# Kernel optimization log

Hardware: AMD Instinct MI355X
Metric: run time of the kernel (lower is better)

Reference implementation:

```python
import jax, jax.numpy as jnp
import numpy as np

B, L, D_MODEL, D_K, HEADS, C = 4, 4096, 512, 64, 8, 2
TOPK = int(C * np.log(L))  # int(c * log(input_seq_len)) = 16


def setup_inputs() -> dict:
    key = jax.random.key(0)
    ks = jax.random.split(key, 5)
    q_in = jax.random.normal(ks[0], (B, L, D_MODEL), jnp.float32)
    k_in = jax.random.normal(ks[1], (B, L, D_MODEL), jnp.float32)
    v_in = jax.random.normal(ks[2], (B, L, D_MODEL), jnp.float32)
    Wq = jax.random.normal(ks[3], (D_MODEL, D_K), jnp.float32) / np.sqrt(D_MODEL)
    bq = jax.random.normal(ks[4], (D_K,), jnp.float32) * 0.01
    return {"q_in": q_in, "k_in": k_in, "v_in": v_in, "Wq": Wq, "bq": bq}


def _to_heads(x, Wq, bq):
    # Faithful to original: ALL of q/k/v use the `query` Dense layer, and all
    # heads are identical copies (same projection stacked `heads` times).
    p = x @ Wq + bq                       # [B, L, d_k]
    p = jnp.swapaxes(p, 1, 2)             # [B, d_k, L]  (transpose [0,3,2,1] of [B,L,d,H])
    return jnp.broadcast_to(p[:, None], (p.shape[0], HEADS, D_K, p.shape[-1]))  # [B,H,d,L]


def reference(q_in, k_in, v_in, Wq, bq):
    Q = jnp.fft.fft(_to_heads(q_in, Wq, bq).astype(jnp.complex64), axis=-1)
    K = jnp.fft.fft(_to_heads(k_in, Wq, bq).astype(jnp.complex64), axis=-1)
    V = _to_heads(v_in, Wq, bq)           # [B,H,d,L] float32
    QK = jnp.fft.ifft(Q * jnp.conj(K), axis=-1)   # circular cross-correlation
    qk_abs = jnp.abs(QK)                  # [B,H,d,L]

    vals, idx = jax.lax.top_k(qk_abs, TOPK)       # [B,H,d,k]
    w = jax.nn.softmax(vals, axis=-1)             # softmax over the k lags

    # tf.roll(v, shift=-lag): out[t] = v[(t + lag) mod L]  -> vectorized gather
    t = jnp.arange(L, dtype=jnp.int32)
    gidx = (idx[..., None] + t) % L               # [B,H,d,k,L]
    Vk = jnp.broadcast_to(V[:, :, :, None, :], gidx.shape)
    rolled = jnp.take_along_axis(Vk, gidx, axis=-1)           # [B,H,d,k,L]
    agg = jnp.sum(rolled * w[..., None], axis=3)              # [B,H,d,L]

    out = agg.reshape(agg.shape[0], HEADS * D_K, L)           # [B, H*d, L]
    return jnp.transpose(out, (0, 2, 1))                      # [B, L, H*d]
```

## Files before the change

kernel.cpp:

```cpp
#include <hip/hip_runtime.h>
#include <hip/hip_bf16.h>

#define BQ 4
#define LQ 4096
#define DM 512
#define DK 64
#define NROWS (BQ * DK)
#define TOPK 16
#define CAND 32

typedef __attribute__((ext_vector_type(4))) float f32x4;
typedef __attribute__((ext_vector_type(8))) short short8v;
typedef __attribute__((ext_vector_type(16))) float f32x16;

__device__ __forceinline__ unsigned short f2bf(float x) {
  unsigned u = __builtin_bit_cast(unsigned, x);
  return (unsigned short)((u + 0x7FFFu + ((u >> 16) & 1u)) >> 16);
}
__device__ __forceinline__ float bf2f(unsigned short h) {
  unsigned u = ((unsigned)h) << 16;
  return __builtin_bit_cast(float, u);
}

__device__ __forceinline__ void gl_lds16(const float* g, float* s) {
  auto g1 = (const __attribute__((address_space(1))) float*)(uintptr_t)g;
  auto s3 = (__attribute__((address_space(3))) float*)(uint32_t)(uintptr_t)s;
  __builtin_amdgcn_global_load_lds(g1, s3, 16, 0, 0);
}

__device__ __forceinline__ void mfma_drain() {
  __builtin_amdgcn_sched_barrier(0);
  asm volatile("s_nop 7\n\ts_nop 7\n\ts_nop 7\n\ts_nop 7" ::: "memory");
  __builtin_amdgcn_sched_barrier(0);
}

#define VMCNT(n)                                            \
  do {                                                      \
    asm volatile("s_waitcnt vmcnt(" #n ")" ::: "memory");   \
    __builtin_amdgcn_sched_barrier(0);                      \
  } while (0)

__global__ __launch_bounds__(256) void wprep_kernel(
    const float* __restrict__ Wq, short* __restrict__ wpack) {
  const int ks = blockIdx.x;
  const int t = threadIdx.x;
  const int lane = t & 63, half = t >> 6;
  const int plane = half >> 1, nt = half & 1;
  const int r = nt * 32 + (lane & 31);
  const int kb = 16 * ks + 8 * (lane >> 5);
  short8v o;
#pragma unroll
  for (int i = 0; i < 8; ++i) {
    float v = Wq[(size_t)(kb + i) * DK + r];
    unsigned short h = f2bf(v);
    o[i] = plane ? (short)f2bf(v - bf2f(h)) : (short)h;
  }
  *(short8v*)(&wpack[(((size_t)plane * 2 + nt) * 32 + ks) * 512 + lane * 8]) = o;
}

#define WLOADR(buf, ksg_)                                                      \
  do {                                                                         \
    const short* wb_ = wp0 + ((size_t)(ksg_) << 9);                            \
    asm volatile("global_load_dwordx4 %0, %1, off" : "=v"(buf[0]) : "v"(wb_)); \
    asm volatile("global_load_dwordx4 %0, %1, off" : "=v"(buf[1]) : "v"(wb_ + (64 << 9))); \
    asm volatile("global_load_dwordx4 %0, %1, off" : "=v"(buf[2]) : "v"(wb_ + (32 << 9))); \
    asm volatile("global_load_dwordx4 %0, %1, off" : "=v"(buf[3]) : "v"(wb_ + (96 << 9))); \
  } while (0)

__global__ __launch_bounds__(256, 2) void proj_kernel(
    const float* __restrict__ q_in, const float* __restrict__ k_in,
    const float* __restrict__ v_in, const short* __restrict__ wpack,
    const float* __restrict__ bq, float* __restrict__ ws) {
  const float* x = blockIdx.z == 0 ? q_in : (blockIdx.z == 1 ? k_in : v_in);
  float* outp = ws + (size_t)blockIdx.z * (size_t)(NROWS * LQ);

  __shared__ __align__(16) float xs[16384];

  const int tid = threadIdx.x;
  const int l = tid & 63, wv = tid >> 6;
  const int r = l & 31, hi = l >> 5;
  const int R0 = blockIdx.x * 32;

  float* slice = xs + wv * 4096;

  {
    const float* xw = x + (size_t)R0 * DM + 128 * wv;
#pragma unroll
    for (int j = 0; j < 16; ++j) {
      const int row = 2 * j + hi;
      const float* src = xw + (size_t)row * DM + ((r ^ (row & 7)) << 2);
      gl_lds16(src, slice + j * 256);
    }
  }

  const short* wp0 = wpack + l * 8;
  short8v wr3[3][4];
  WLOADR(wr3[0], 8 * wv + 0);
  WLOADR(wr3[1], 8 * wv + 1);

  f32x16 acc[2];
#pragma unroll
  for (int nt = 0; nt < 2; ++nt)
#pragma unroll
    for (int i = 0; i < 16; ++i) acc[nt][i] = 0.f;

  const float* rbase = slice + r * 128;
  const int c = r & 7;

#pragma unroll
  for (int kl = 0; kl < 8; ++kl) {
    if (kl < 6) WLOADR(wr3[(kl + 2) % 3], 8 * wv + kl + 2);
    if (kl < 6) VMCNT(8);
    else if (kl == 6) VMCNT(4);
    else VMCNT(0);

    const int q0 = 4 * kl + 2 * hi;
    f32x4 xa = *(const f32x4*)(rbase + ((q0 ^ c) << 2));
    f32x4 xb2 = *(const f32x4*)(rbase + (((q0 + 1) ^ c) << 2));
    float f[8] = {xa[0], xa[1], xa[2], xa[3], xb2[0], xb2[1], xb2[2], xb2[3]};
    short8v ah, al;
#pragma unroll
    for (int i = 0; i < 8; ++i) {
      unsigned short h = f2bf(f[i]);
      ah[i] = (short)h;
      al[i] = (short)f2bf(f[i] - bf2f(h));
    }
    short8v* w_ = wr3[kl % 3];
    asm volatile(
        "s_nop 4\n\t"
        "v_mfma_f32_32x32x16_bf16 %0, %2, %4, %0\n\t"
        "v_mfma_f32_32x32x16_bf16 %0, %2, %5, %0\n\t"
        "v_mfma_f32_32x32x16_bf16 %0, %3, %4, %0\n\t"
        "v_mfma_f32_32x32x16_bf16 %1, %2, %6, %1\n\t"
        "v_mfma_f32_32x32x16_bf16 %1, %2, %7, %1\n\t"
        "v_mfma_f32_32x32x16_bf16 %1, %3, %6, %1\n\t"
        "s_nop 7\n\t"
        "s_nop 3"
        : "+v"(acc[0]), "+v"(acc[1])
        : "v"(ah), "v"(al), "v"(w_[0]), "v"(w_[1]), "v"(w_[2]), "v"(w_[3]));
  }

  mfma_drain();
#pragma unroll
  for (int nt = 0; nt < 2; ++nt)
#pragma unroll
    for (int rr = 0; rr < 16; ++rr)
      slice[nt * 1024 + rr * 64 + l] = acc[nt][rr];
  __syncthreads();

  if (wv < 2) {
    const int nt = wv;
    float sacc[16];
#pragma unroll
    for (int rr = 0; rr < 16; ++rr)
      sacc[rr] = xs[0 * 4096 + nt * 1024 + rr * 64 + l] +
                 xs[1 * 4096 + nt * 1024 + rr * 64 + l] +
                 xs[2 * 4096 + nt * 1024 + rr * 64 + l] +
                 xs[3 * 4096 + nt * 1024 + rr * 64 + l];
    float* area = xs + wv * 4096 + 2048;
    const float bb = bq[nt * 32 + r];
#pragma unroll
    for (int rr = 0; rr < 16; ++rr) {
      int io = (rr & 3) + 8 * (rr >> 2) + 4 * hi;
      area[r * 34 + io] = sacc[rr] + bb;
    }
    asm volatile("s_waitcnt lgkmcnt(0)" ::: "memory");
    __builtin_amdgcn_sched_barrier(0);
    const int e = l & 15, jg = l >> 4;
    const int b = R0 >> 12, i0 = R0 & (LQ - 1);
#pragma unroll
    for (int p = 0; p < 8; ++p) {
      int jj = jg * 8 + p;
      float2 v = *reinterpret_cast<const float2*>(area + jj * 34 + e * 2);
      *reinterpret_cast<float2*>(
          &outp[((size_t)b * DK + nt * 32 + jj) * LQ + i0 + e * 2]) = v;
    }
  }
}

__global__ __launch_bounds__(512) void corr_topk_kernel(
    const float* __restrict__ qp, const float* __restrict__ kp,
    float* __restrict__ lw) {
  const int row = blockIdx.x;
  const int tid = threadIdx.x;
  __shared__ __align__(16) short qs[3 * 4112 + 4096];
  __shared__ __align__(16) short ks[4096];
  __shared__ __align__(16) float qf[LQ];
  __shared__ __align__(16) float kf[LQ];
  __shared__ unsigned wk[128];
  __shared__ unsigned scand[CAND];
  __shared__ float rS[CAND];
  __shared__ float ordv[TOPK]; __shared__ int ordl[TOPK];

  const float* qr = qp + ((size_t)row << 12);
  const float* kr = kp + ((size_t)row << 12);

  {
    const float4* q4 = (const float4*)qr;
    float4 v0 = q4[tid * 2], v1 = q4[tid * 2 + 1];
    float4 v2 = q4[(tid * 2 + 2) & 1023];
    ((float4*)qf)[tid * 2] = v0;
    ((float4*)qf)[tid * 2 + 1] = v1;
    float f[12] = {v0.x, v0.y, v0.z, v0.w, v1.x, v1.y, v1.z, v1.w,
                   v2.x, v2.y, v2.z, v2.w};
#pragma unroll
    for (int r = 0; r < 4; ++r) {
      short8v o;
#pragma unroll
      for (int i = 0; i < 8; ++i) o[i] = (short)f2bf(f[i + r]);
      *(short8v*)(&qs[r * 4112 + tid * 8]) = o;
    }
    const float4* k4 = (const float4*)kr;
    float4 w0 = k4[tid * 2], w1 = k4[tid * 2 + 1];
    ((float4*)kf)[tid * 2] = w0;
    ((float4*)kf)[tid * 2 + 1] = w1;
    float g[8] = {w0.x, w0.y, w0.z, w0.w, w1.x, w1.y, w1.z, w1.w};
    int Q = tid;
    int Qs = Q ^ ((Q >> 3) & 7);
    short8v o;
#pragma unroll
    for (int i = 0; i < 8; ++i) o[i] = (short)f2bf(g[i]);
    *(short8v*)(&ks[Qs << 3]) = o;
  }
  __syncthreads();

  const int l = tid & 63, wv = tid >> 6;
  const int Oq = ((8 * (l >> 5) - 32 * (l & 31)) & 4095) >> 3;
  const int rB = (l & 31) & 3;
  const int Ce = (l & 31) + 8 * (l >> 5) - rB;
  const short* qb = qs + rB * 4112;

  f32x16 acc[4];
#pragma unroll
  for (int M = 0; M < 4; ++M)
#pragma unroll
    for (int i = 0; i < 16; ++i) acc[M][i] = 0.f;

  const int J0 = wv * 32;
#pragma unroll 2
  for (int jb = 0; jb < 32; ++jb) {
    const int J = J0 + jb;
    int e1 = (Ce + 16 * J) & 4095;
    int e2 = (e1 + 4) & 4095;
    uint2 blo = *(const uint2*)(qb + e1);
    uint2 bhi = *(const uint2*)(qb + e2);
    int4 bi; bi.x = blo.x; bi.y = blo.y; bi.z = bhi.x; bi.w = bhi.y;
    short8v bf = __builtin_bit_cast(short8v, bi);
    const int Dq = 2 * J;
#pragma unroll
    for (int M = 0; M < 4; ++M) {
      int Q = (Oq + Dq - 128 * M) & 511;
      Q ^= (Q >> 3) & 7;
      short8v af = *(const short8v*)(&ks[Q << 3]);
      asm volatile("v_mfma_f32_32x32x16_bf16 %0, %1, %2, %0"
                   : "+v"(acc[M]) : "v"(af), "v"(bf));
    }
  }

  mfma_drain();
  __syncthreads();
  float* red = (float*)qs;
  const int strip = (wv & 1) * 4096;
  const int ch4 = (l >> 5) * 4, cn = l & 31;
#define RIDX(M, r) (strip + ((M) << 10) + 32 * (((r)&3) + 8 * ((r) >> 2) + ch4) + cn)
  if (wv < 2) {
#pragma unroll
    for (int M = 0; M < 4; ++M)
#pragma unroll
      for (int r = 0; r < 16; ++r) red[RIDX(M, r)] = acc[M][r];
  }
  __syncthreads();
  if (wv >= 2 && wv < 4) {
#pragma unroll
    for (int M = 0; M < 4; ++M)
#pragma unroll
      for (int r = 0; r < 16; ++r) red[RIDX(M, r)] += acc[M][r];
  }
  __syncthreads();
  if (wv >= 4 && wv < 6) {
#pragma unroll
    for (int M = 0; M < 4; ++M)
#pragma unroll
      for (int r = 0; r < 16; ++r) red[RIDX(M, r)] += acc[M][r];
  }
  __syncthreads();
  if (wv >= 6) {
#pragma unroll
    for (int M = 0; M < 4; ++M)
#pragma unroll
      for (int r = 0; r < 16; ++r) red[RIDX(M, r)] += acc[M][r];
  }
  __syncthreads();
#undef RIDX

  {
    unsigned key[8];
#pragma unroll
    for (int i = 0; i < 8; ++i) {
      int tau = wv * 512 + i * 64 + l;
      float v = red[tau] + red[4096 + tau];
      unsigned u = __builtin_bit_cast(unsigned, fabsf(v));
      key[i] = (u & 0xFFFFF000u) | (unsigned)(4095 - tau);
    }
    unsigned bkey = key[0];
#pragma unroll
    for (int i = 1; i < 8; ++i) bkey = key[i] > bkey ? key[i] : bkey;
    for (int round = 0; round < 16; ++round) {
      unsigned m = bkey;
#pragma unroll
      for (int off = 1; off < 64; off <<= 1) {
        unsigned o = __shfl_xor(m, off);
        m = o > m ? o : m;
      }
      if (l == 0) wk[wv * 16 + round] = m;
#pragma unroll
      for (int i = 0; i < 8; ++i) key[i] = (key[i] == m) ? 0u : key[i];
      bkey = key[0];
#pragma unroll
      for (int i = 1; i < 8; ++i) bkey = key[i] > bkey ? key[i] : bkey;
    }
  }
  __syncthreads();

  if (tid < 128) {
    unsigned ki = wk[tid];
    int rank = 0;
    for (int j = 0; j < 128; ++j) rank += (wk[j] > ki);
    if (rank < CAND) scand[rank] = ki;
  }
  __syncthreads();

  {
    const int ci = tid >> 4, sub = tid & 15;
    const int lag = 4095 - (int)(scand[ci] & 0xFFFu);
    float S0 = 0.f, S1 = 0.f, S2 = 0.f, S3 = 0.f;
    for (int it = 0; it < 256; it += 4) {
      int t0 = (it + 0) * 16 + sub, t1 = (it + 1) * 16 + sub;
      int t2 = (it + 2) * 16 + sub, t3 = (it + 3) * 16 + sub;
      S0 = fmaf(kf[t0], qf[(t0 + lag) & 4095], S0);
      S1 = fmaf(kf[t1], qf[(t1 + lag) & 4095], S1);
      S2 = fmaf(kf[t2], qf[(t2 + lag) & 4095], S2);
      S3 = fmaf(kf[t3], qf[(t3 + lag) & 4095], S3);
    }
    float S = (S0 + S1) + (S2 + S3);
    S += __shfl_xor(S, 1);
    S += __shfl_xor(S, 2);
    S += __shfl_xor(S, 4);
    S += __shfl_xor(S, 8);
    if (sub == 0) rS[ci] = S;
  }
  __syncthreads();

  if (tid < CAND) {
    float vi = fabsf(rS[tid]);
    int ii = 4095 - (int)(scand[tid] & 0xFFFu);
    int rank = 0;
    for (int j = 0; j < CAND; ++j) {
      float vj = fabsf(rS[j]);
      int ij = 4095 - (int)(scand[j] & 0xFFFu);
      rank += (vj > vi) || (vj == vi && ij < ii);
    }
    if (rank < TOPK) { ordv[rank] = vi; ordl[rank] = ii; }
  }
  __syncthreads();

  if (tid == 0) {
    float m0 = ordv[0], s = 0.f, e[TOPK];
    for (int k = 0; k < TOPK; ++k) { e[k] = expf(ordv[k] - m0); s += e[k]; }
    float inv = 1.f / s;
    int* ip = (int*)(lw + (size_t)row * 32);
    for (int k = 0; k < TOPK; ++k) {
      ip[k] = ordl[k];
      ((float*)ip)[TOPK + k] = e[k] * inv;
    }
  }
}

__global__ void agg_kernel(const float* __restrict__ vpT,
                           const float* __restrict__ lw,
                           float* __restrict__ aggT) {
  const int row = blockIdx.x, tid = threadIdx.x;
  __shared__ __align__(16) float vr[2 * LQ];
  __shared__ float w[TOPK]; __shared__ int lg[TOPK];

  const float* v0 = vpT + (size_t)row * LQ;
  for (int x = tid; x < LQ; x += 256) {
    float val = v0[x];
    vr[x] = val; vr[x + LQ] = val;
  }
  if (tid < TOPK) {
    lg[tid] = ((const int*)(lw + (size_t)row * 32))[tid];
    w[tid] = lw[(size_t)row * 32 + TOPK + tid];
  }
  __syncthreads();

  float wr[TOPK]; int lr[TOPK];
#pragma unroll
  for (int k = 0; k < TOPK; ++k) { wr[k] = w[k]; lr[k] = lg[k]; }

  for (int m = 0; m < 16; ++m) {
    int t = m * 256 + tid;
    float a = 0.f;
#pragma unroll
    for (int k = 0; k < TOPK; ++k) a = fmaf(wr[k], vr[t + lr[k]], a);
    aggT[(size_t)row * LQ + t] = a;
  }
}

__global__ void trans_kernel(const float* __restrict__ aggT,
                             float* __restrict__ out) {
  const int b = blockIdx.y;
  const int t0 = blockIdx.x * 64;
  const int tid = threadIdx.x;
  __shared__ float ts[64][65];

#pragma unroll
  for (int v = 0; v < 16; ++v) {
    int f = v * 256 + tid;
    int d = f >> 6, tt = f & 63;
    ts[d][tt] = aggT[((size_t)b * DK + d) * LQ + t0 + tt];
  }
  __syncthreads();

#pragma unroll
  for (int v = 0; v < 128; ++v) {
    int f = v * 256 + tid;
    int tt = f >> 9, c = f & 511;
    out[((size_t)b * LQ + t0 + tt) * (8 * DK) + c] = ts[c & 63][tt];
  }
}

extern "C" void kernel_launch(void* const* d_in, const int* in_sizes, int n_in,
                              void* d_out, int out_size, void* d_ws, size_t ws_size,
                              hipStream_t stream) {
  const float* q_in = (const float*)d_in[0];
  const float* k_in = (const float*)d_in[1];
  const float* v_in = (const float*)d_in[2];
  const float* Wq   = (const float*)d_in[3];
  const float* bq   = (const float*)d_in[4];
  float* out = (float*)d_out;
  float* ws  = (float*)d_ws;

  const size_t M = (size_t)NROWS * LQ;
  float* qp    = ws;
  float* kp    = ws + M;
  float* vp    = ws + 2 * M;
  float* lw    = ws + 3 * M;
  float* aggT  = ws + 4 * M;
  short* wpack = (short*)(ws + 5 * M);

  wprep_kernel<<<32, 256, 0, stream>>>(Wq, wpack);
  proj_kernel<<<dim3(512, 1, 3), 256, 0, stream>>>(q_in, k_in, v_in, wpack,
                                                   bq, ws);
  corr_topk_kernel<<<NROWS, 512, 0, stream>>>(qp, kp, lw);
  agg_kernel<<<NROWS, 256, 0, stream>>>(vp, lw, aggT);
  trans_kernel<<<dim3(LQ / 64, BQ), 256, 0, stream>>>(aggT, out);
}
```

Measured before the change: 77.34 us.

## Fold V projection into correlation/top-k kernel as extra blocks

Moves the V projection out of the projection kernel and runs it as 512 extra blocks of the correlation/top-k launch, which otherwise has only 256 blocks (one per row). The projection body becomes a shared device function, and shared memory is carved from one union buffer. The aim is to fill idle CUs during the latency-bound correlation phase and drop a third of the projection launch's work. In exchange, the V-projection blocks idle half their threads and reserve the full 75 KB of LDS. The tighter 512-thread, 2-blocks-per-CU launch bound may also cap registers for the correlation code and cause spills.

After: 75.65 us. -2.2%, faster.

```diff
diff --git a/kernel.cpp b/kernel.cpp
--- a/kernel.cpp
+++ b/kernel.cpp
@@ -67,20 +67,12 @@
     asm volatile("global_load_dwordx4 %0, %1, off" : "=v"(buf[3]) : "v"(wb_ + (96 << 9))); \
   } while (0)
 
-__global__ __launch_bounds__(256, 2) void proj_kernel(
-    const float* __restrict__ q_in, const float* __restrict__ k_in,
-    const float* __restrict__ v_in, const short* __restrict__ wpack,
-    const float* __restrict__ bq, float* __restrict__ ws) {
-  const float* x = blockIdx.z == 0 ? q_in : (blockIdx.z == 1 ? k_in : v_in);
-  float* outp = ws + (size_t)blockIdx.z * (size_t)(NROWS * LQ);
-
-  __shared__ __align__(16) float xs[16384];
-
-  const int tid = threadIdx.x;
+__device__ __forceinline__ void proj_tile_body(
+    const float* __restrict__ x, const short* __restrict__ wpack,
+    const float* __restrict__ bq, float* __restrict__ outp, int R0,
+    float* xs, int tid) {
   const int l = tid & 63, wv = tid >> 6;
   const int r = l & 31, hi = l >> 5;
-  const int R0 = blockIdx.x * 32;
-
   float* slice = xs + wv * 4096;
 
   {
@@ -178,19 +170,41 @@
   }
 }
 
-__global__ __launch_bounds__(512) void corr_topk_kernel(
+__global__ __launch_bounds__(256, 2) void proj_kernel(
+    const float* __restrict__ q_in, const float* __restrict__ k_in,
+    const short* __restrict__ wpack, const float* __restrict__ bq,
+    float* __restrict__ ws) {
+  __shared__ __align__(16) float xs[16384];
+  const float* x = blockIdx.z == 0 ? q_in : k_in;
+  float* outp = ws + (size_t)blockIdx.z * (size_t)(NROWS * LQ);
+  proj_tile_body(x, wpack, bq, outp, blockIdx.x * 32, xs, threadIdx.x);
+}
+
+__global__ __launch_bounds__(512, 2) void corr_projv_kernel(
     const float* __restrict__ qp, const float* __restrict__ kp,
+    const float* __restrict__ v_in, const short* __restrict__ wpack,
+    const float* __restrict__ bq, float* __restrict__ vp,
     float* __restrict__ lw) {
+  __shared__ __align__(16) char smem_u[76800];
+  const int tid = threadIdx.x;
+
+  if (blockIdx.x >= 256) {
+    if (tid >= 256) return;
+    proj_tile_body(v_in, wpack, bq, vp, (blockIdx.x - 256) * 32,
+                   (float*)smem_u, tid);
+    return;
+  }
+
   const int row = blockIdx.x;
-  const int tid = threadIdx.x;
-  __shared__ __align__(16) short qs[3 * 4112 + 4096];
-  __shared__ __align__(16) short ks[4096];
-  __shared__ __align__(16) float qf[LQ];
-  __shared__ __align__(16) float kf[LQ];
-  __shared__ unsigned wk[128];
-  __shared__ unsigned scand[CAND];
-  __shared__ float rS[CAND];
-  __shared__ float ordv[TOPK]; __shared__ int ordl[TOPK];
+  short* qs = (short*)smem_u;
+  short* ks = (short*)(smem_u + 32864);
+  float* qf = (float*)(smem_u + 41056);
+  float* kf = (float*)(smem_u + 57440);
+  unsigned* wk = (unsigned*)(smem_u + 73824);
+  unsigned* scand = (unsigned*)(smem_u + 74336);
+  float* rS = (float*)(smem_u + 74464);
+  float* ordv = (float*)(smem_u + 74592);
+  int* ordl = (int*)(smem_u + 74656);
 
   const float* qr = qp + ((size_t)row << 12);
   const float* kr = kp + ((size_t)row << 12);
@@ -450,9 +464,8 @@
   short* wpack = (short*)(ws + 5 * M);
 
   wprep_kernel<<<32, 256, 0, stream>>>(Wq, wpack);
-  proj_kernel<<<dim3(512, 1, 3), 256, 0, stream>>>(q_in, k_in, v_in, wpack,
-                                                   bq, ws);
-  corr_topk_kernel<<<NROWS, 512, 0, stream>>>(qp, kp, lw);
+  proj_kernel<<<dim3(512, 1, 2), 256, 0, stream>>>(q_in, k_in, wpack, bq, ws);
+  corr_projv_kernel<<<768, 512, 0, stream>>>(qp, kp, v_in, wpack, bq, vp, lw);
   agg_kernel<<<NROWS, 256, 0, stream>>>(vp, lw, aggT);
   trans_kernel<<<dim3(LQ / 64, BQ), 256, 0, stream>>>(aggT, out);
 }
```
